# Optimization experiments

Measured on AMD Instinct MI355X. Metric: run time of the kernel, lower is better.

The kernel has to match this reference:

```python
import jax, jax.numpy as jnp
import numpy as np

GRID = (32, 32)
LATENT = 256
ALPHA = 1.0
DECAY = 0.9


def _cdist(a, b):
    # Euclidean pairwise distance with a grad-safe sqrt (0 where d2==0, like torch.cdist).
    d2 = jnp.sum(a * a, -1)[:, None] + jnp.sum(b * b, -1)[None, :] - 2.0 * (a @ b.T)
    d2 = jnp.maximum(d2, 0.0)
    mask = d2 > 0
    return jnp.where(mask, jnp.sqrt(jnp.where(mask, d2, 1.0)), 0.0)


def setup_inputs() -> dict:
    key = jax.random.key(0)
    k1, k2 = jax.random.split(key)
    z = jax.random.normal(k1, (64, 512, 256), dtype=jnp.float32)
    nodes = jax.random.normal(k2, (GRID[0], GRID[1], LATENT), dtype=jnp.float32)
    return {"z": z, "nodes": nodes}


def reference(z, nodes):
    b, t, d = z.shape
    # time_decay^(seq_len - t - 1)
    tw = DECAY ** (t - 1 - jnp.arange(t, dtype=jnp.float32))
    z_flat = (z * tw[None, :, None]).reshape(b * t, d)   # (b t) d
    nodes_flat = nodes.reshape(-1, d)                     # n d

    dist = _cdist(z_flat, nodes_flat)                     # (b t) n
    q = 1.0 / (1.0 + dist / ALPHA) ** ((ALPHA + 1.0) / 2.0)
    q = q / jnp.sum(q, axis=-1, keepdims=True)            # L1 normalize rows
    q2 = q * q
    p = q2 / jnp.sum(q2, axis=0, keepdims=True)
    p = p / jnp.sum(p, axis=-1, keepdims=True)

    bmu = jnp.argmin(dist, axis=-1).reshape(b, t)         # int32

    # F.kl_div(q.log(), p, reduction='batchmean') = sum(p*(log p - log q)) / N
    kl_loss = jnp.sum(p * (jnp.log(p) - jnp.log(q))) / (b * t)
    diversity_loss = -jnp.mean(_cdist(nodes_flat, nodes_flat))
    time_smooth_loss = jnp.mean((z[:, 1:] - z[:, :-1]) ** 2) * DECAY

    # vectorized neighborhood consistency (python loop in the original is an
    # unweighted mean over all (b, t) adjacent pairs since seq_len is uniform)
    gw = GRID[1]
    pc = jnp.stack([bmu[:, :-1] // gw, bmu[:, :-1] % gw], axis=-1)
    nc = jnp.stack([bmu[:, 1:] // gw, bmu[:, 1:] % gw], axis=-1)
    neighbor_loss = jnp.mean(jnp.sum(jnp.abs(pc - nc), axis=-1).astype(jnp.float32))

    total_loss = kl_loss + 0.5 * diversity_loss + 0.3 * time_smooth_loss + 0.2 * neighbor_loss

    bmu_nodes = nodes_flat[bmu.reshape(-1)].reshape(b, t, d)
    som_z = z + 0.1 * (bmu_nodes - z)
    return (som_z, total_loss, kl_loss, diversity_loss, time_smooth_loss, neighbor_loss, q, bmu)
```

## Files before the change

### kernel.cpp

```cpp
#include <hip/hip_runtime.h>
#include <math.h>

#define Bb 64
#define Tt 512
#define Dd 256
#define Nn 1024
#define NROWS 32768

#define OUT_SOM 0L
#define OUT_SCAL 8388608L
#define OUT_Q 8388613L
#define OUT_BMU 41943045L

typedef __attribute__((ext_vector_type(8))) short bf16x8;
typedef __attribute__((ext_vector_type(4))) float f32x4;
typedef unsigned long long u64;
typedef unsigned short ushortT;

static __device__ __forceinline__ unsigned short f2bf(float x) {
  unsigned int u = __float_as_uint(x);
  unsigned int r = (u + 0x7fffu + ((u >> 16) & 1u)) >> 16;
  return (unsigned short)r;
}
static __device__ __forceinline__ float bf2f(unsigned short b) {
  return __uint_as_float(((unsigned int)b) << 16);
}

static __device__ __forceinline__ float block_reduce_sum(float v, float* sb) {
#pragma unroll
  for (int o = 32; o > 0; o >>= 1) v += __shfl_down(v, o, 64);
  const int lane = threadIdx.x & 63, w = threadIdx.x >> 6;
  if (lane == 0) sb[w] = v;
  __syncthreads();
  return (threadIdx.x == 0) ? (sb[0] + sb[1] + sb[2] + sb[3]) : 0.0f;
}

__global__ __launch_bounds__(256) void k_conv(
    const float* __restrict__ z, const float* __restrict__ nodes,
    ushortT* __restrict__ zhiF, ushortT* __restrict__ zloF, float* __restrict__ zn,
    ushortT* __restrict__ nhiF, ushortT* __restrict__ nloF, float* __restrict__ nnorm) {
  __shared__ float sm[32 * 260];
  const int tid = threadIdx.x;
  if (blockIdx.x < 1024) {
    const int rt = blockIdx.x;
    const long row0 = (long)rt * 32;
    const int r = tid >> 3, c8 = tid & 7;
    const long rowg = row0 + r;
    const int t = (int)(rowg & (Tt - 1));
    const float tw = powf(0.9f, (float)(Tt - 1 - t));
    float nrm = 0.f;
#pragma unroll
    for (int k = 0; k < 8; ++k) {
      const int c4 = c8 + k * 8;
      float4 v = ((const float4*)(z + rowg * Dd))[c4];
      v.x *= tw; v.y *= tw; v.z *= tw; v.w *= tw;
      *(float4*)&sm[r * 260 + c4 * 4] = v;
      nrm += v.x * v.x + v.y * v.y + v.z * v.z + v.w * v.w;
    }
    nrm += __shfl_xor(nrm, 1, 64);
    nrm += __shfl_xor(nrm, 2, 64);
    nrm += __shfl_xor(nrm, 4, 64);
    if (c8 == 0) zn[rowg] = nrm;
    __syncthreads();
    ushort4* oh = (ushort4*)(zhiF + (long)rt * 8192);
    ushort4* ol = (ushort4*)(zloF + (long)rt * 8192);
#pragma unroll
    for (int i = 0; i < 8; ++i) {
      const int o4 = tid + 256 * i;
      const int e4 = (o4 & 1) * 4;
      const int r16 = (o4 >> 1) & 15;
      const int k8 = (o4 >> 5) & 3;
      const int g = (o4 >> 7) & 1;
      const int ks = o4 >> 8;
      const float* p = &sm[(g * 16 + r16) * 260 + ks * 32 + k8 * 8 + e4];
      const float4 v = *(const float4*)p;
      ushort4 h, l;
      h.x = f2bf(v.x); l.x = f2bf(v.x - bf2f(h.x));
      h.y = f2bf(v.y); l.y = f2bf(v.y - bf2f(h.y));
      h.z = f2bf(v.z); l.z = f2bf(v.z - bf2f(h.z));
      h.w = f2bf(v.w); l.w = f2bf(v.w - bf2f(h.w));
      oh[o4] = h;
      ol[o4] = l;
    }
  } else {
    const int ct = blockIdx.x - 1024;
    const int jr = tid >> 4, cg = tid & 15;
    const long nrow = (long)(ct * 16 + jr);
    float nrm = 0.f;
#pragma unroll
    for (int k = 0; k < 4; ++k) {
      const int c4 = cg + k * 16;
      const float4 v = ((const float4*)(nodes + nrow * Dd))[c4];
      *(float4*)&sm[jr * 260 + c4 * 4] = v;
      nrm += v.x * v.x + v.y * v.y + v.z * v.z + v.w * v.w;
    }
    nrm += __shfl_xor(nrm, 1, 64);
    nrm += __shfl_xor(nrm, 2, 64);
    nrm += __shfl_xor(nrm, 4, 64);
    nrm += __shfl_xor(nrm, 8, 64);
    if (cg == 0) nnorm[nrow] = nrm;
    __syncthreads();
    ushort4* oh = (ushort4*)(nhiF + (long)ct * 4096);
    ushort4* ol = (ushort4*)(nloF + (long)ct * 4096);
#pragma unroll
    for (int i = 0; i < 4; ++i) {
      const int o4 = tid + 256 * i;
      const int e4 = (o4 & 1) * 4;
      const int c16 = (o4 >> 1) & 15;
      const int k8 = (o4 >> 5) & 3;
      const int ks = o4 >> 7;
      const float* p = &sm[c16 * 260 + ks * 32 + k8 * 8 + e4];
      const float4 v = *(const float4*)p;
      ushort4 h, l;
      h.x = f2bf(v.x); l.x = f2bf(v.x - bf2f(h.x));
      h.y = f2bf(v.y); l.y = f2bf(v.y - bf2f(h.y));
      h.z = f2bf(v.z); l.z = f2bf(v.z - bf2f(h.z));
      h.w = f2bf(v.w); l.w = f2bf(v.w - bf2f(h.w));
      oh[o4] = h;
      ol[o4] = l;
    }
  }
}

__global__ __launch_bounds__(512, 2) void k_gemm3(
    const ushortT* __restrict__ zhiF, const ushortT* __restrict__ zloF,
    const ushortT* __restrict__ nhiF, const ushortT* __restrict__ nloF,
    const float* __restrict__ zn, const float* __restrict__ nn,
    float* __restrict__ qout, float* __restrict__ bmuf, float* __restrict__ colsum) {
  __shared__ float srowS[64][8];
  __shared__ u64 sbmu[64][8];
  __shared__ float sinv[64];
  const int tid = threadIdx.x, lane = tid & 63, w = tid >> 6;
  const int rl = lane & 15, kq = lane >> 4;
  const long row0 = (long)blockIdx.x * 64;

  const ushortT* Ah0 = zhiF + (long)blockIdx.x * 16384;
  const ushortT* Al0 = zloF + (long)blockIdx.x * 16384;
  const ushortT* Bh = nhiF + (long)w * 8 * 4096;
  const ushortT* Bl = nloF + (long)w * 8 * 4096;
  const int lo8 = lane * 8;

  f32x4 acc[2][2][8];
#pragma unroll
  for (int rg = 0; rg < 2; ++rg)
#pragma unroll
    for (int g = 0; g < 2; ++g)
#pragma unroll
      for (int c = 0; c < 8; ++c) acc[rg][g][c] = (f32x4){0.f, 0.f, 0.f, 0.f};

#pragma unroll 1
  for (int ks = 0; ks < 8; ++ks) {
    bf16x8 ah[2][2], al[2][2];
#pragma unroll
    for (int rg = 0; rg < 2; ++rg)
#pragma unroll
      for (int g = 0; g < 2; ++g) {
        ah[rg][g] = *(const bf16x8*)(Ah0 + rg * 8192 + (ks * 2 + g) * 512 + lo8);
        al[rg][g] = *(const bf16x8*)(Al0 + rg * 8192 + (ks * 2 + g) * 512 + lo8);
      }
#pragma unroll
    for (int c = 0; c < 8; ++c) {
      const bf16x8 bh = *(const bf16x8*)(Bh + c * 4096 + ks * 512 + lo8);
      const bf16x8 bl = *(const bf16x8*)(Bl + c * 4096 + ks * 512 + lo8);
      __builtin_amdgcn_s_setprio(1);
#pragma unroll
      for (int rg = 0; rg < 2; ++rg)
#pragma unroll
        for (int g = 0; g < 2; ++g) {
          acc[rg][g][c] = __builtin_amdgcn_mfma_f32_16x16x32_bf16(ah[rg][g], bh, acc[rg][g][c], 0, 0, 0);
          acc[rg][g][c] = __builtin_amdgcn_mfma_f32_16x16x32_bf16(ah[rg][g], bl, acc[rg][g][c], 0, 0, 0);
          acc[rg][g][c] = __builtin_amdgcn_mfma_f32_16x16x32_bf16(al[rg][g], bh, acc[rg][g][c], 0, 0, 0);
        }
      __builtin_amdgcn_s_setprio(0);
    }
  }

  float nnv[8];
#pragma unroll
  for (int c = 0; c < 8; ++c) nnv[c] = nn[w * 128 + c * 16 + rl];

#pragma unroll
  for (int rg = 0; rg < 2; ++rg) {
    float rs[2][4];
    u64 bm[2][4];
#pragma unroll
    for (int g = 0; g < 2; ++g)
#pragma unroll
      for (int r = 0; r < 4; ++r) {
        rs[g][r] = 0.f;
        bm[g][r] = ~0ull;
      }
#pragma unroll
    for (int g = 0; g < 2; ++g) {
      float znv[4];
#pragma unroll
      for (int r = 0; r < 4; ++r) znv[r] = zn[row0 + rg * 32 + g * 16 + kq * 4 + r];
#pragma unroll
      for (int c = 0; c < 8; ++c)
#pragma unroll
        for (int r = 0; r < 4; ++r) {
          const float dot = acc[rg][g][c][r];
          const float d2 = znv[r] + nnv[c] - 2.f * dot;
          const float dist = sqrtf(fmaxf(d2, 0.f));
          const float qv = 1.f / (1.f + dist);
          acc[rg][g][c][r] = qv;
          rs[g][r] += qv;
          const int col = w * 128 + c * 16 + rl;
          const u64 pk = ((u64)__float_as_uint(dist) << 32) | (unsigned int)col;
          bm[g][r] = pk < bm[g][r] ? pk : bm[g][r];
        }
    }
#pragma unroll
    for (int g = 0; g < 2; ++g)
#pragma unroll
      for (int r = 0; r < 4; ++r) {
#pragma unroll
        for (int m = 1; m < 16; m <<= 1) {
          rs[g][r] += __shfl_xor(rs[g][r], m, 64);
          const u64 o = __shfl_xor(bm[g][r], m, 64);
          bm[g][r] = o < bm[g][r] ? o : bm[g][r];
        }
        if (rl == 0) {
          srowS[rg * 32 + g * 16 + kq * 4 + r][w] = rs[g][r];
          sbmu[rg * 32 + g * 16 + kq * 4 + r][w] = bm[g][r];
        }
      }
  }
  __syncthreads();
  if (tid < 64) {
    float s = 0.f;
    u64 best = ~0ull;
#pragma unroll
    for (int i = 0; i < 8; ++i) {
      s += srowS[tid][i];
      const u64 v = sbmu[tid][i];
      best = v < best ? v : best;
    }
    sinv[tid] = 1.f / s;
    bmuf[row0 + tid] = (float)(int)(unsigned int)(best & 0xffffffffull);
  }
  __syncthreads();

  float cp[8];
#pragma unroll
  for (int c = 0; c < 8; ++c) cp[c] = 0.f;
#pragma unroll
  for (int rg = 0; rg < 2; ++rg)
#pragma unroll
    for (int g = 0; g < 2; ++g) {
      float inv[4];
#pragma unroll
      for (int r = 0; r < 4; ++r) inv[r] = sinv[rg * 32 + g * 16 + kq * 4 + r];
#pragma unroll
      for (int c = 0; c < 8; ++c)
#pragma unroll
        for (int r = 0; r < 4; ++r) {
          const float qn = acc[rg][g][c][r] * inv[r];
          qout[(row0 + rg * 32 + g * 16 + kq * 4 + r) * Nn + w * 128 + c * 16 + rl] = qn;
          cp[c] = fmaf(qn, qn, cp[c]);
        }
    }
#pragma unroll
  for (int c = 0; c < 8; ++c) {
    cp[c] += __shfl_xor(cp[c], 16, 64);
    cp[c] += __shfl_xor(cp[c], 32, 64);
    if (kq == 0) atomicAdd(&colsum[w * 128 + c * 16 + rl], cp[c]);
  }
}

__global__ __launch_bounds__(256) void k_div2(
    const ushortT* __restrict__ nhiF, const ushortT* __restrict__ nloF,
    const float* __restrict__ nnorm, float* __restrict__ scal) {
  __shared__ float sb[4];
  const int tid = threadIdx.x, lane = tid & 63, w = tid >> 6;
  const int rl = lane & 15, kq = lane >> 4;
  const int bi = blockIdx.x & 63;
  const int cq = blockIdx.x >> 6;
  const int lo8 = lane * 8;

  f32x4 acc[4];
#pragma unroll
  for (int c = 0; c < 4; ++c) acc[c] = (f32x4){0.f, 0.f, 0.f, 0.f};

#pragma unroll 1
  for (int ks = 0; ks < 8; ++ks) {
    const bf16x8 ah = *(const bf16x8*)(nhiF + (long)bi * 4096 + ks * 512 + lo8);
    const bf16x8 al = *(const bf16x8*)(nloF + (long)bi * 4096 + ks * 512 + lo8);
#pragma unroll
    for (int c = 0; c < 4; ++c) {
      const long ct = (long)(cq * 16 + w * 4 + c);
      const bf16x8 bh = *(const bf16x8*)(nhiF + ct * 4096 + ks * 512 + lo8);
      const bf16x8 bl = *(const bf16x8*)(nloF + ct * 4096 + ks * 512 + lo8);
      acc[c] = __builtin_amdgcn_mfma_f32_16x16x32_bf16(ah, bh, acc[c], 0, 0, 0);
      acc[c] = __builtin_amdgcn_mfma_f32_16x16x32_bf16(ah, bl, acc[c], 0, 0, 0);
      acc[c] = __builtin_amdgcn_mfma_f32_16x16x32_bf16(al, bh, acc[c], 0, 0, 0);
    }
  }
  float ni[4];
#pragma unroll
  for (int r = 0; r < 4; ++r) ni[r] = nnorm[bi * 16 + kq * 4 + r];
  float dsum = 0.f;
#pragma unroll
  for (int c = 0; c < 4; ++c) {
    const float nj = nnorm[(cq * 16 + w * 4 + c) * 16 + rl];
#pragma unroll
    for (int r = 0; r < 4; ++r) {
      const float d2 = ni[r] + nj - 2.f * acc[c][r];
      dsum += sqrtf(fmaxf(d2, 0.f));
    }
  }
  const float tot = block_reduce_sum(dsum, sb);
  if (tid == 0) atomicAdd(&scal[1], tot);
}

__global__ __launch_bounds__(256) void k_kl(const float* __restrict__ q,
                                            const float* __restrict__ colsum,
                                            float* __restrict__ scal) {
  __shared__ float rcs[Nn];
  __shared__ float lcs[Nn];
  __shared__ float sb[4];
  const int tid = threadIdx.x, lane = tid & 63, wave = tid >> 6;
#pragma unroll
  for (int j = 0; j < 4; ++j) {
    const float cs = colsum[tid + 256 * j];
    rcs[tid + 256 * j] = 1.f / cs;
    lcs[tid + 256 * j] = __logf(cs);
  }
  __syncthreads();
  const long r0 = (long)blockIdx.x * 16;
  float klp = 0.f;
  for (int rr = 0; rr < 4; ++rr) {
    const long row = r0 + rr * 4 + wave;
    float s = 0.f, a = 0.f;
#pragma unroll
    for (int j = 0; j < 16; ++j) {
      const int col = lane + 64 * j;
      const float t = q[row * Nn + col];
      const float u = t * t * rcs[col];
      s += u;
      a = fmaf(u, __logf(t) - lcs[col], a);
    }
#pragma unroll
    for (int o = 1; o < 64; o <<= 1) {
      s += __shfl_xor(s, o, 64);
      a += __shfl_xor(a, o, 64);
    }
    if (lane == 0) klp += a / s - __logf(s);
  }
  const float tot = block_reduce_sum(klp, sb);
  if (tid == 0) atomicAdd(&scal[0], tot);
}

__global__ __launch_bounds__(256) void k_somnb(const float* __restrict__ z,
                                               const float* __restrict__ nodes,
                                               const float* __restrict__ bmuf,
                                               float* __restrict__ som,
                                               float* __restrict__ scal) {
  __shared__ float sb[4];
  const int tid = threadIdx.x;
  const long r0 = (long)blockIdx.x * 16;
  float ts = 0.f, zp = 0.f;
  if ((r0 & (Tt - 1)) > 0) zp = z[(r0 - 1) * Dd + tid];
  for (int r = 0; r < 16; ++r) {
    const long row = r0 + r;
    const float zc = z[row * Dd + tid];
    const int bi = (int)bmuf[row];
    const float nv = nodes[(long)bi * Dd + tid];
    som[row * Dd + tid] = zc + 0.1f * (nv - zc);
    if ((row & (Tt - 1)) > 0) {
      const float dd = zc - zp;
      ts = fmaf(dd, dd, ts);
    }
    zp = zc;
  }
  const float tts = block_reduce_sum(ts, sb);
  if (tid == 0) atomicAdd(&scal[2], tts);
  float nbv = 0.f;
  if (tid < 16) {
    const long row = r0 + tid;
    if ((row & (Tt - 1)) != (Tt - 1)) {
      const int b1 = (int)bmuf[row], b2 = (int)bmuf[row + 1];
      nbv = (float)(abs((b1 >> 5) - (b2 >> 5)) + abs((b1 & 31) - (b2 & 31)));
    }
  }
  __syncthreads();
  const float tnb = block_reduce_sum(nbv, sb);
  if (tid == 0) atomicAdd(&scal[3], tnb);
}

__global__ void k_final(const float* __restrict__ scal, float* __restrict__ o) {
  const float kl = scal[0] * (1.f / 32768.f);
  const float dv = -scal[1] * (1.f / (1024.f * 1024.f));
  const float ts = scal[2] * (0.9f / (64.f * 511.f * 256.f));
  const float nb = scal[3] * (1.f / 32704.f);
  o[0] = kl + 0.5f * dv + 0.3f * ts + 0.2f * nb;
  o[1] = kl;
  o[2] = dv;
  o[3] = ts;
  o[4] = nb;
}

__global__ __launch_bounds__(256) void k_prep_fb(const float* __restrict__ nodes,
                                                 float* __restrict__ nt,
                                                 float* __restrict__ nnorm) {
  __shared__ float sb[4];
  const int j = blockIdx.x, d = threadIdx.x;
  const float v = nodes[j * Dd + d];
  nt[(long)d * Nn + j] = v;
  const float tot = block_reduce_sum(v * v, sb);
  if (threadIdx.x == 0) nnorm[j] = tot;
}

__global__ __launch_bounds__(256) void k_div_fb(const float* __restrict__ nodes,
                                                const float* __restrict__ nt,
                                                const float* __restrict__ nnorm,
                                                float* __restrict__ scal) {
  __shared__ float ni[4][Dd];
  __shared__ float sb[4];
  const int tid = threadIdx.x;
  const int i0 = blockIdx.x * 4;
#pragma unroll
  for (int r = 0; r < 4; ++r) ni[r][tid] = nodes[(i0 + r) * Dd + tid];
  __syncthreads();
  float acc[4][4];
#pragma unroll
  for (int r = 0; r < 4; ++r)
#pragma unroll
    for (int jj = 0; jj < 4; ++jj) acc[r][jj] = 0.f;
  for (int d = 0; d < Dd; ++d) {
    float nj[4];
#pragma unroll
    for (int jj = 0; jj < 4; ++jj) nj[jj] = nt[(long)d * Nn + tid + 256 * jj];
#pragma unroll
    for (int r = 0; r < 4; ++r) {
      const float s = ni[r][d];
#pragma unroll
      for (int jj = 0; jj < 4; ++jj) acc[r][jj] = fmaf(s, nj[jj], acc[r][jj]);
    }
  }
  float sum = 0.f;
#pragma unroll
  for (int r = 0; r < 4; ++r)
#pragma unroll
    for (int jj = 0; jj < 4; ++jj) {
      const float d2 = nnorm[i0 + r] + nnorm[tid + 256 * jj] - 2.f * acc[r][jj];
      sum += sqrtf(fmaxf(d2, 0.f));
    }
  const float tot = block_reduce_sum(sum, sb);
  if (tid == 0) atomicAdd(&scal[1], tot);
}

__global__ __launch_bounds__(256) void k_dist_fb(
    const float* __restrict__ z, const float* __restrict__ nt,
    const float* __restrict__ nnorm, float* __restrict__ qout,
    float* __restrict__ srow, float* __restrict__ bmuf) {
  __shared__ float zt[Dd][65];
  __shared__ float rs4[4][64];
  __shared__ u64 cand[4][64];
  const int tid = threadIdx.x, lane = tid & 63, wave = tid >> 6;
  const long row0 = (long)blockIdx.x * 64;
  for (int k = 0; k < 64; ++k) {
    const int t = (int)((row0 + k) & (Tt - 1));
    const float tw = powf(0.9f, (float)(Tt - 1 - t));
    zt[tid][k] = z[(row0 + k) * Dd + tid] * tw;
  }
  __syncthreads();
  float zns = 0.f;
  for (int d = 0; d < Dd; ++d) {
    const float v = zt[d][lane];
    zns = fmaf(v, v, zns);
  }
  const long myrow = row0 + lane;
  float rsum = 0.f;
  u64 best = ~0ull;
  const int j0w = wave * 256;
  for (int chunk = 0; chunk < 16; ++chunk) {
    const int j0 = j0w + chunk * 16;
    float acc[16];
#pragma unroll
    for (int i = 0; i < 16; ++i) acc[i] = 0.f;
    const float* ntp = nt + j0;
    for (int d = 0; d < Dd; ++d) {
      const float zv = zt[d][lane];
      const float4 a = ((const float4*)ntp)[0];
      const float4 b = ((const float4*)ntp)[1];
      const float4 c = ((const float4*)ntp)[2];
      const float4 e = ((const float4*)ntp)[3];
      ntp += Nn;
      acc[0] = fmaf(zv, a.x, acc[0]); acc[1] = fmaf(zv, a.y, acc[1]);
      acc[2] = fmaf(zv, a.z, acc[2]); acc[3] = fmaf(zv, a.w, acc[3]);
      acc[4] = fmaf(zv, b.x, acc[4]); acc[5] = fmaf(zv, b.y, acc[5]);
      acc[6] = fmaf(zv, b.z, acc[6]); acc[7] = fmaf(zv, b.w, acc[7]);
      acc[8] = fmaf(zv, c.x, acc[8]); acc[9] = fmaf(zv, c.y, acc[9]);
      acc[10] = fmaf(zv, c.z, acc[10]); acc[11] = fmaf(zv, c.w, acc[11]);
      acc[12] = fmaf(zv, e.x, acc[12]); acc[13] = fmaf(zv, e.y, acc[13]);
      acc[14] = fmaf(zv, e.z, acc[14]); acc[15] = fmaf(zv, e.w, acc[15]);
    }
#pragma unroll
    for (int jj = 0; jj < 16; ++jj) {
      const int j = j0 + jj;
      const float d2 = zns + nnorm[j] - 2.f * acc[jj];
      const float dist = sqrtf(fmaxf(d2, 0.f));
      const float qr = 1.f / (1.f + dist);
      qout[myrow * Nn + j] = qr;
      rsum += qr;
      const u64 pk = ((u64)__float_as_uint(dist) << 32) | (unsigned int)j;
      best = pk < best ? pk : best;
    }
  }
  rs4[wave][lane] = rsum;
  cand[wave][lane] = best;
  __syncthreads();
  if (wave == 0) {
    const float s = rs4[0][lane] + rs4[1][lane] + rs4[2][lane] + rs4[3][lane];
    srow[myrow] = s;
    const u64 m0 = cand[0][lane] < cand[1][lane] ? cand[0][lane] : cand[1][lane];
    const u64 m1 = cand[2][lane] < cand[3][lane] ? cand[2][lane] : cand[3][lane];
    const u64 m = m0 < m1 ? m0 : m1;
    bmuf[myrow] = (float)(int)(unsigned int)(m & 0xffffffffull);
  }
}

__global__ __launch_bounds__(256) void k_norm_fb(float* __restrict__ q,
                                                 const float* __restrict__ srow,
                                                 float* __restrict__ colsum) {
  const int tid = threadIdx.x;
  const long r0 = (long)blockIdx.x * 16;
  float cs[4] = {0.f, 0.f, 0.f, 0.f};
  for (int r = 0; r < 16; ++r) {
    const long row = r0 + r;
    const float inv = 1.f / srow[row];
#pragma unroll
    for (int j = 0; j < 4; ++j) {
      const long idx = row * Nn + tid + 256 * j;
      const float v = q[idx] * inv;
      q[idx] = v;
      cs[j] = fmaf(v, v, cs[j]);
    }
  }
#pragma unroll
  for (int j = 0; j < 4; ++j) atomicAdd(&colsum[tid + 256 * j], cs[j]);
}

extern "C" void kernel_launch(void* const* d_in, const int* in_sizes, int n_in,
                              void* d_out, int out_size, void* d_ws, size_t ws_size,
                              hipStream_t stream) {
  const float* z = (const float*)d_in[0];
  const float* nodes = (const float*)d_in[1];
  float* out = (float*)d_out;
  unsigned char* ws = (unsigned char*)d_ws;

  float* som = out + OUT_SOM;
  float* scal_out = out + OUT_SCAL;
  float* qout = out + OUT_Q;
  float* bmuf = out + OUT_BMU;

  const size_t NEED = 34742288;
  if (ws_size >= NEED) {
    ushortT* zhiF = (ushortT*)(ws + 0);
    ushortT* zloF = (ushortT*)(ws + 16777216);
    ushortT* nhiF = (ushortT*)(ws + 33554432);
    ushortT* nloF = (ushortT*)(ws + 34078720);
    float* zn = (float*)(ws + 34603008);
    float* nnorm = (float*)(ws + 34734080);
    float* colsum = (float*)(ws + 34738176);
    float* scal = (float*)(ws + 34742272);

    hipMemsetAsync(colsum, 0, 4096 + 16, stream);

    k_conv<<<1088, 256, 0, stream>>>(z, nodes, zhiF, zloF, zn, nhiF, nloF, nnorm);
    k_gemm3<<<512, 512, 0, stream>>>(zhiF, zloF, nhiF, nloF, zn, nnorm, qout, bmuf, colsum);
    k_div2<<<256, 256, 0, stream>>>(nhiF, nloF, nnorm, scal);
    k_kl<<<2048, 256, 0, stream>>>(qout, colsum, scal);
    k_somnb<<<2048, 256, 0, stream>>>(z, nodes, bmuf, som, scal);
    k_final<<<1, 1, 0, stream>>>(scal, scal_out);
  } else {
    float* wsf = (float*)ws;
    float* nt = wsf;
    float* nnorm = wsf + 262144;
    float* srow = wsf + 263168;
    float* colsum = wsf + 295936;
    float* scal = wsf + 296960;

    hipMemsetAsync(colsum, 0, (1024 + 4) * sizeof(float), stream);
    k_prep_fb<<<1024, 256, 0, stream>>>(nodes, nt, nnorm);
    k_div_fb<<<256, 256, 0, stream>>>(nodes, nt, nnorm, scal);
    k_dist_fb<<<512, 256, 0, stream>>>(z, nt, nnorm, qout, srow, bmuf);
    k_norm_fb<<<2048, 256, 0, stream>>>(qout, srow, colsum);
    k_kl<<<2048, 256, 0, stream>>>(qout, colsum, scal);
    k_somnb<<<2048, 256, 0, stream>>>(z, nodes, bmuf, som, scal);
    k_final<<<1, 1, 0, stream>>>(scal, scal_out);
  }
}
```

Measured before the change: 249.9 us.

## Retile distance GEMM into 32-row blocks of 16 waves and vectorise KL loads

The fused distance/softmax GEMM kernel is retiled from 64-row blocks with 8 waves (8 column tiles each) to 32-row blocks with 16 waves (4 column tiles each), launched as 1024 blocks of 1024 threads. All B fragments for a k-step are loaded before issuing the MFMAs, and the k-loop is unrolled by two. The aim is higher occupancy and fewer accumulator registers per thread, at the cost of more cross-wave reduction work and twice as many colsum atomics. The KL kernel now reads q with float4 loads and float4 shared-memory tables, and the diversity kernel's k-loop is also unrolled by two.

```diff
diff --git a/kernel.cpp b/kernel.cpp
--- a/kernel.cpp
+++ b/kernel.cpp
@@ -122,116 +122,110 @@
   }
 }
 
-__global__ __launch_bounds__(512, 2) void k_gemm3(
+__global__ __launch_bounds__(1024, 4) void k_gemm4(
     const ushortT* __restrict__ zhiF, const ushortT* __restrict__ zloF,
     const ushortT* __restrict__ nhiF, const ushortT* __restrict__ nloF,
     const float* __restrict__ zn, const float* __restrict__ nn,
     float* __restrict__ qout, float* __restrict__ bmuf, float* __restrict__ colsum) {
-  __shared__ float srowS[64][8];
-  __shared__ u64 sbmu[64][8];
-  __shared__ float sinv[64];
+  __shared__ float srowS[32][16];
+  __shared__ u64 sbmu[32][16];
+  __shared__ float sinv[32];
   const int tid = threadIdx.x, lane = tid & 63, w = tid >> 6;
   const int rl = lane & 15, kq = lane >> 4;
-  const long row0 = (long)blockIdx.x * 64;
-
-  const ushortT* Ah0 = zhiF + (long)blockIdx.x * 16384;
-  const ushortT* Al0 = zloF + (long)blockIdx.x * 16384;
-  const ushortT* Bh = nhiF + (long)w * 8 * 4096;
-  const ushortT* Bl = nloF + (long)w * 8 * 4096;
+  const int rt = blockIdx.x;
+  const long row0 = (long)rt * 32;
+
+  const ushortT* Ah = zhiF + (long)rt * 8192;
+  const ushortT* Al = zloF + (long)rt * 8192;
+  const ushortT* Bh = nhiF + (long)w * 4 * 4096;
+  const ushortT* Bl = nloF + (long)w * 4 * 4096;
   const int lo8 = lane * 8;
 
-  f32x4 acc[2][2][8];
-#pragma unroll
-  for (int rg = 0; rg < 2; ++rg)
-#pragma unroll
-    for (int g = 0; g < 2; ++g)
-#pragma unroll
-      for (int c = 0; c < 8; ++c) acc[rg][g][c] = (f32x4){0.f, 0.f, 0.f, 0.f};
-
-#pragma unroll 1
+  f32x4 acc[2][4];
+#pragma unroll
+  for (int g = 0; g < 2; ++g)
+#pragma unroll
+    for (int c = 0; c < 4; ++c) acc[g][c] = (f32x4){0.f, 0.f, 0.f, 0.f};
+
+#pragma unroll 2
   for (int ks = 0; ks < 8; ++ks) {
-    bf16x8 ah[2][2], al[2][2];
-#pragma unroll
-    for (int rg = 0; rg < 2; ++rg)
+    bf16x8 ah[2], al[2], bh[4], bl[4];
+#pragma unroll
+    for (int g = 0; g < 2; ++g) {
+      ah[g] = *(const bf16x8*)(Ah + (ks * 2 + g) * 512 + lo8);
+      al[g] = *(const bf16x8*)(Al + (ks * 2 + g) * 512 + lo8);
+    }
+#pragma unroll
+    for (int c = 0; c < 4; ++c) {
+      bh[c] = *(const bf16x8*)(Bh + c * 4096 + ks * 512 + lo8);
+      bl[c] = *(const bf16x8*)(Bl + c * 4096 + ks * 512 + lo8);
+    }
+    __builtin_amdgcn_s_setprio(1);
+#pragma unroll
+    for (int c = 0; c < 4; ++c)
 #pragma unroll
       for (int g = 0; g < 2; ++g) {
-        ah[rg][g] = *(const bf16x8*)(Ah0 + rg * 8192 + (ks * 2 + g) * 512 + lo8);
-        al[rg][g] = *(const bf16x8*)(Al0 + rg * 8192 + (ks * 2 + g) * 512 + lo8);
+        acc[g][c] = __builtin_amdgcn_mfma_f32_16x16x32_bf16(ah[g], bh[c], acc[g][c], 0, 0, 0);
+        acc[g][c] = __builtin_amdgcn_mfma_f32_16x16x32_bf16(ah[g], bl[c], acc[g][c], 0, 0, 0);
+        acc[g][c] = __builtin_amdgcn_mfma_f32_16x16x32_bf16(al[g], bh[c], acc[g][c], 0, 0, 0);
       }
-#pragma unroll
-    for (int c = 0; c < 8; ++c) {
-      const bf16x8 bh = *(const bf16x8*)(Bh + c * 4096 + ks * 512 + lo8);
-      const bf16x8 bl = *(const bf16x8*)(Bl + c * 4096 + ks * 512 + lo8);
-      __builtin_amdgcn_s_setprio(1);
-#pragma unroll
-      for (int rg = 0; rg < 2; ++rg)
-#pragma unroll
-        for (int g = 0; g < 2; ++g) {
-          acc[rg][g][c] = __builtin_amdgcn_mfma_f32_16x16x32_bf16(ah[rg][g], bh, acc[rg][g][c], 0, 0, 0);
-          acc[rg][g][c] = __builtin_amdgcn_mfma_f32_16x16x32_bf16(ah[rg][g], bl, acc[rg][g][c], 0, 0, 0);
-          acc[rg][g][c] = __builtin_amdgcn_mfma_f32_16x16x32_bf16(al[rg][g], bh, acc[rg][g][c], 0, 0, 0);
-        }
-      __builtin_amdgcn_s_setprio(0);
-    }
-  }
-
-  float nnv[8];
-#pragma unroll
-  for (int c = 0; c < 8; ++c) nnv[c] = nn[w * 128 + c * 16 + rl];
-
-#pragma unroll
-  for (int rg = 0; rg < 2; ++rg) {
-    float rs[2][4];
-    u64 bm[2][4];
-#pragma unroll
-    for (int g = 0; g < 2; ++g)
+    __builtin_amdgcn_s_setprio(0);
+  }
+
+  float nnv[4];
+#pragma unroll
+  for (int c = 0; c < 4; ++c) nnv[c] = nn[w * 64 + c * 16 + rl];
+
+  float rs[2][4];
+  u64 bm[2][4];
+#pragma unroll
+  for (int g = 0; g < 2; ++g)
+#pragma unroll
+    for (int r = 0; r < 4; ++r) {
+      rs[g][r] = 0.f;
+      bm[g][r] = ~0ull;
+    }
+#pragma unroll
+  for (int g = 0; g < 2; ++g) {
+    float znv[4];
+#pragma unroll
+    for (int r = 0; r < 4; ++r) znv[r] = zn[row0 + g * 16 + kq * 4 + r];
+#pragma unroll
+    for (int c = 0; c < 4; ++c)
 #pragma unroll
       for (int r = 0; r < 4; ++r) {
-        rs[g][r] = 0.f;
-        bm[g][r] = ~0ull;
+        const float dot = acc[g][c][r];
+        const float d2 = znv[r] + nnv[c] - 2.f * dot;
+        const float dist = sqrtf(fmaxf(d2, 0.f));
+        const float qv = 1.f / (1.f + dist);
+        acc[g][c][r] = qv;
+        rs[g][r] += qv;
+        const int col = w * 64 + c * 16 + rl;
+        const u64 pk = ((u64)__float_as_uint(dist) << 32) | (unsigned int)col;
+        bm[g][r] = pk < bm[g][r] ? pk : bm[g][r];
       }
-#pragma unroll
-    for (int g = 0; g < 2; ++g) {
-      float znv[4];
-#pragma unroll
-      for (int r = 0; r < 4; ++r) znv[r] = zn[row0 + rg * 32 + g * 16 + kq * 4 + r];
-#pragma unroll
-      for (int c = 0; c < 8; ++c)
-#pragma unroll
-        for (int r = 0; r < 4; ++r) {
-          const float dot = acc[rg][g][c][r];
-          const float d2 = znv[r] + nnv[c] - 2.f * dot;
-          const float dist = sqrtf(fmaxf(d2, 0.f));
-          const float qv = 1.f / (1.f + dist);
-          acc[rg][g][c][r] = qv;
-          rs[g][r] += qv;
-          const int col = w * 128 + c * 16 + rl;
-          const u64 pk = ((u64)__float_as_uint(dist) << 32) | (unsigned int)col;
-          bm[g][r] = pk < bm[g][r] ? pk : bm[g][r];
-        }
-    }
-#pragma unroll
-    for (int g = 0; g < 2; ++g)
-#pragma unroll
-      for (int r = 0; r < 4; ++r) {
-#pragma unroll
-        for (int m = 1; m < 16; m <<= 1) {
-          rs[g][r] += __shfl_xor(rs[g][r], m, 64);
-          const u64 o = __shfl_xor(bm[g][r], m, 64);
-          bm[g][r] = o < bm[g][r] ? o : bm[g][r];
-        }
-        if (rl == 0) {
-          srowS[rg * 32 + g * 16 + kq * 4 + r][w] = rs[g][r];
-          sbmu[rg * 32 + g * 16 + kq * 4 + r][w] = bm[g][r];
-        }
+  }
+#pragma unroll
+  for (int g = 0; g < 2; ++g)
+#pragma unroll
+    for (int r = 0; r < 4; ++r) {
+#pragma unroll
+      for (int m = 1; m < 16; m <<= 1) {
+        rs[g][r] += __shfl_xor(rs[g][r], m, 64);
+        const u64 o = __shfl_xor(bm[g][r], m, 64);
+        bm[g][r] = o < bm[g][r] ? o : bm[g][r];
       }
-  }
-  __syncthreads();
-  if (tid < 64) {
+      if (rl == 0) {
+        srowS[g * 16 + kq * 4 + r][w] = rs[g][r];
+        sbmu[g * 16 + kq * 4 + r][w] = bm[g][r];
+      }
+    }
+  __syncthreads();
+  if (tid < 32) {
     float s = 0.f;
     u64 best = ~0ull;
 #pragma unroll
-    for (int i = 0; i < 8; ++i) {
+    for (int i = 0; i < 16; ++i) {
       s += srowS[tid][i];
       const u64 v = sbmu[tid][i];
       best = v < best ? v : best;
@@ -241,30 +235,28 @@
   }
   __syncthreads();
 
-  float cp[8];
-#pragma unroll
-  for (int c = 0; c < 8; ++c) cp[c] = 0.f;
-#pragma unroll
-  for (int rg = 0; rg < 2; ++rg)
-#pragma unroll
-    for (int g = 0; g < 2; ++g) {
-      float inv[4];
-#pragma unroll
-      for (int r = 0; r < 4; ++r) inv[r] = sinv[rg * 32 + g * 16 + kq * 4 + r];
-#pragma unroll
-      for (int c = 0; c < 8; ++c)
-#pragma unroll
-        for (int r = 0; r < 4; ++r) {
-          const float qn = acc[rg][g][c][r] * inv[r];
-          qout[(row0 + rg * 32 + g * 16 + kq * 4 + r) * Nn + w * 128 + c * 16 + rl] = qn;
-          cp[c] = fmaf(qn, qn, cp[c]);
-        }
-    }
-#pragma unroll
-  for (int c = 0; c < 8; ++c) {
+  float cp[4];
+#pragma unroll
+  for (int c = 0; c < 4; ++c) cp[c] = 0.f;
+#pragma unroll
+  for (int g = 0; g < 2; ++g) {
+    float inv[4];
+#pragma unroll
+    for (int r = 0; r < 4; ++r) inv[r] = sinv[g * 16 + kq * 4 + r];
+#pragma unroll
+    for (int c = 0; c < 4; ++c)
+#pragma unroll
+      for (int r = 0; r < 4; ++r) {
+        const float qn = acc[g][c][r] * inv[r];
+        qout[(row0 + g * 16 + kq * 4 + r) * Nn + w * 64 + c * 16 + rl] = qn;
+        cp[c] = fmaf(qn, qn, cp[c]);
+      }
+  }
+#pragma unroll
+  for (int c = 0; c < 4; ++c) {
     cp[c] += __shfl_xor(cp[c], 16, 64);
     cp[c] += __shfl_xor(cp[c], 32, 64);
-    if (kq == 0) atomicAdd(&colsum[w * 128 + c * 16 + rl], cp[c]);
+    if (kq == 0) atomicAdd(&colsum[w * 64 + c * 16 + rl], cp[c]);
   }
 }
 
@@ -282,7 +274,7 @@
 #pragma unroll
   for (int c = 0; c < 4; ++c) acc[c] = (f32x4){0.f, 0.f, 0.f, 0.f};
 
-#pragma unroll 1
+#pragma unroll 2
   for (int ks = 0; ks < 8; ++ks) {
     const bf16x8 ah = *(const bf16x8*)(nhiF + (long)bi * 4096 + ks * 512 + lo8);
     const bf16x8 al = *(const bf16x8*)(nloF + (long)bi * 4096 + ks * 512 + lo8);
@@ -316,15 +308,17 @@
 __global__ __launch_bounds__(256) void k_kl(const float* __restrict__ q,
                                             const float* __restrict__ colsum,
                                             float* __restrict__ scal) {
-  __shared__ float rcs[Nn];
-  __shared__ float lcs[Nn];
+  __shared__ float4 rcs4[Nn / 4];
+  __shared__ float4 lcs4[Nn / 4];
   __shared__ float sb[4];
   const int tid = threadIdx.x, lane = tid & 63, wave = tid >> 6;
-#pragma unroll
-  for (int j = 0; j < 4; ++j) {
-    const float cs = colsum[tid + 256 * j];
-    rcs[tid + 256 * j] = 1.f / cs;
-    lcs[tid + 256 * j] = __logf(cs);
+  {
+    const float c0 = colsum[tid * 4 + 0];
+    const float c1 = colsum[tid * 4 + 1];
+    const float c2 = colsum[tid * 4 + 2];
+    const float c3 = colsum[tid * 4 + 3];
+    rcs4[tid] = make_float4(1.f / c0, 1.f / c1, 1.f / c2, 1.f / c3);
+    lcs4[tid] = make_float4(__logf(c0), __logf(c1), __logf(c2), __logf(c3));
   }
   __syncthreads();
   const long r0 = (long)blockIdx.x * 16;
@@ -333,12 +327,16 @@
     const long row = r0 + rr * 4 + wave;
     float s = 0.f, a = 0.f;
 #pragma unroll
-    for (int j = 0; j < 16; ++j) {
-      const int col = lane + 64 * j;
-      const float t = q[row * Nn + col];
-      const float u = t * t * rcs[col];
-      s += u;
-      a = fmaf(u, __logf(t) - lcs[col], a);
+    for (int j = 0; j < 4; ++j) {
+      const int c4 = lane + 64 * j;
+      const float4 qv = *(const float4*)(q + row * Nn + c4 * 4);
+      const float4 rc = rcs4[c4];
+      const float4 lc = lcs4[c4];
+      float u;
+      u = qv.x * qv.x * rc.x; s += u; a = fmaf(u, __logf(qv.x) - lc.x, a);
+      u = qv.y * qv.y * rc.y; s += u; a = fmaf(u, __logf(qv.y) - lc.y, a);
+      u = qv.z * qv.z * rc.z; s += u; a = fmaf(u, __logf(qv.z) - lc.z, a);
+      u = qv.w * qv.w * rc.w; s += u; a = fmaf(u, __logf(qv.w) - lc.w, a);
     }
 #pragma unroll
     for (int o = 1; o < 64; o <<= 1) {
@@ -569,7 +567,7 @@
     hipMemsetAsync(colsum, 0, 4096 + 16, stream);
 
     k_conv<<<1088, 256, 0, stream>>>(z, nodes, zhiF, zloF, zn, nhiF, nloF, nnorm);
-    k_gemm3<<<512, 512, 0, stream>>>(zhiF, zloF, nhiF, nloF, zn, nnorm, qout, bmuf, colsum);
+    k_gemm4<<<1024, 1024, 0, stream>>>(zhiF, zloF, nhiF, nloF, zn, nnorm, qout, bmuf, colsum);
     k_div2<<<256, 256, 0, stream>>>(nhiF, nloF, nnorm, scal);
     k_kl<<<2048, 256, 0, stream>>>(qout, colsum, scal);
     k_somnb<<<2048, 256, 0, stream>>>(z, nodes, bmuf, som, scal);
```

Result: no change. 251.6 us (+0.7%).
